# Performance work log

Measured on AMD Instinct MI355X. Metric: run time of the kernel, lower is better.

Reference implementation:

```python
import jax, jax.numpy as jnp
import numpy as np

N_NODES = 100_000
N_EDGES = 3_200_000
D_IN, D_EDGE, D_HID, D_OUT = 8, 4, 32, 16
NEG_SLOPE = 0.2  # PyG GATv2Conv default


def setup_inputs() -> dict:
    key = jax.random.key(0)
    ks = jax.random.split(key, 13)
    s = 0.1
    return {
        "x": jax.random.normal(ks[0], (N_NODES, D_IN), jnp.float32),
        "edge_index": jax.random.randint(ks[1], (2, N_EDGES), 0, N_NODES, dtype=jnp.int64),
        "edge_attr": jax.random.normal(ks[2], (N_EDGES, D_EDGE), jnp.float32),
        "Wl1": jax.random.normal(ks[3], (D_IN, D_HID), jnp.float32) * s,
        "Wr1": jax.random.normal(ks[4], (D_IN, D_HID), jnp.float32) * s,
        "We1": jax.random.normal(ks[5], (D_EDGE, D_HID), jnp.float32) * s,
        "att1": jax.random.normal(ks[6], (D_HID,), jnp.float32) * s,
        "b1": jnp.zeros((D_HID,), jnp.float32),
        "Wl2": jax.random.normal(ks[7], (D_HID, D_OUT), jnp.float32) * s,
        "Wr2": jax.random.normal(ks[8], (D_HID, D_OUT), jnp.float32) * s,
        "We2": jax.random.normal(ks[9], (D_EDGE, D_OUT), jnp.float32) * s,
        "att2": jax.random.normal(ks[10], (D_OUT,), jnp.float32) * s,
        "b2": jnp.zeros((D_OUT,), jnp.float32),
    }


def _segment_softmax(score, seg, n):
    m = jax.ops.segment_max(score, seg, num_segments=n)
    e = jnp.exp(score - m[seg])
    z = jax.ops.segment_sum(e, seg, num_segments=n)
    return e / z[seg]


def _gatv2(x, src, dst, ea_raw, Wl, Wr, We, att, bias, n):
    # GATv2 (heads=1): score_ij = att . leaky_relu(Wl x_j + Wr x_i + We e_ij)
    xl = x @ Wl            # [N, d]
    xr = x @ Wr            # [N, d]
    ea = ea_raw @ We       # [E, d]
    h = jax.nn.leaky_relu(xl[src] + xr[dst] + ea, NEG_SLOPE)  # [E, d]
    score = h @ att        # [E]
    alpha = _segment_softmax(score, dst, n)
    out = jax.ops.segment_sum(alpha[:, None] * xl[src], dst, num_segments=n)
    return out + bias


def reference(x, edge_index, edge_attr, Wl1, Wr1, We1, att1, b1, Wl2, Wr2, We2, att2, b2):
    n = x.shape[0]
    src, dst = edge_index[0], edge_index[1]
    # add_self_loops=True with fill_value='mean': self-loop edge_attr = mean of
    # incoming raw edge_attr per target node (0 for isolated targets)
    ones = jnp.ones((src.shape[0],), x.dtype)
    cnt = jax.ops.segment_sum(ones, dst, num_segments=n)
    loop_attr = jax.ops.segment_sum(edge_attr, dst, num_segments=n) / jnp.maximum(cnt, 1.0)[:, None]
    ar = jnp.arange(n, dtype=src.dtype)
    src2 = jnp.concatenate([src, ar])
    dst2 = jnp.concatenate([dst, ar])
    ea2 = jnp.concatenate([edge_attr, loop_attr], axis=0)
    h = jax.nn.relu(_gatv2(x, src2, dst2, ea2, Wl1, Wr1, We1, att1, b1, n))
    out = _gatv2(h, src2, dst2, ea2, Wl2, Wr2, We2, att2, b2, n)
    return out.reshape(-1)
```

## Files before the change

kernel.cpp:

```cpp
#include <hip/hip_runtime.h>

#define NEG_SLOPE 0.2f
#define CHUNK 16384
#define KMAX  1600
#define CAP   3264
#define NBLKMAX 256

__global__ __launch_bounds__(1024) void k_bin(const int* __restrict__ ei,
                                              const float* __restrict__ eattr,
                                              int* __restrict__ cloff,
                                              int* __restrict__ ssrc,
                                              float4* __restrict__ seat,
                                              int E, int K) {
    __shared__ int s_off[KMAX + 1];
    __shared__ unsigned s_eid[CHUNK];
    int t = threadIdx.x;
    for (int i = t; i <= K; i += 1024) s_off[i] = 0;
    __syncthreads();
    int base = blockIdx.x * CHUNK;
    int end = min(base + CHUNK, E);
    int Ec = end - base;
    unsigned pack[CHUNK / 1024];
#pragma unroll
    for (int i = 0; i < CHUNK / 1024; i++) {
        int el = t + 1024 * i;
        pack[i] = 0xFFFFFFFFu;
        if (el < Ec) {
            int dst = ei[E + base + el];
            int b = dst >> 6;
            int r = atomicAdd(&s_off[b], 1);
            pack[i] = ((unsigned)b << 20) | ((unsigned)(dst & 63) << 14) | (unsigned)r;
        }
    }
    __syncthreads();
    if (t < 64) {
        int run = 0;
        for (int bb = 0; bb < K; bb += 64) {
            int b = bb + t;
            int v = (b < K) ? s_off[b] : 0;
            int x = v;
#pragma unroll
            for (int off = 1; off < 64; off <<= 1) {
                int y = __shfl_up(x, off, 64);
                if (t >= off) x += y;
            }
            if (b < K) s_off[b] = run + x - v;
            run += __shfl(x, 63, 64);
        }
        if (t == 0) s_off[K] = run;
    }
    __syncthreads();
#pragma unroll
    for (int i = 0; i < CHUNK / 1024; i++) {
        int el = t + 1024 * i;
        if (el < Ec) {
            unsigned p = pack[i];
            int b = p >> 20;
            int r = p & 0x3FFF;
            int dl = (p >> 14) & 63;
            s_eid[s_off[b] + r] = ((unsigned)dl << 14) | (unsigned)el;
        }
    }
    __syncthreads();
    for (int pos = t; pos < Ec; pos += 1024) {
        unsigned v = s_eid[pos];
        int el = v & 0x3FFF;
        int dl = v >> 14;
        int e = base + el;
        int src = ei[e];
        float4 a = *(const float4*)(eattr + 4ll * e);
        ssrc[base + pos] = src | (dl << 17);
        seat[base + pos] = a;
    }
    for (int i = t; i <= K; i += 1024)
        cloff[(long long)blockIdx.x * (K + 1) + i] = s_off[i];
}

__global__ void k_transp(const int* __restrict__ in, int* __restrict__ out, int R, int C) {
    __shared__ int tile[32][33];
    int c0 = blockIdx.x * 32, r0 = blockIdx.y * 32;
    int c = c0 + threadIdx.x, r = r0 + threadIdx.y;
    if (r < R && c < C) tile[threadIdx.y][threadIdx.x] = in[(long long)r * C + c];
    __syncthreads();
    int oc = r0 + threadIdx.x, orr = c0 + threadIdx.y;
    if (orr < C && oc < R) out[(long long)orr * R + oc] = tile[threadIdx.x][threadIdx.y];
}

__global__ void k_btot(const int* __restrict__ cloffT, int* __restrict__ bucketTotal,
                       int K, int NBLK) {
    int b = (blockIdx.x * blockDim.x + threadIdx.x) >> 6;
    int lane = threadIdx.x & 63;
    if (b >= K) return;
    const int* r0 = cloffT + (long long)b * NBLK;
    const int* r1 = r0 + NBLK;
    int s = 0;
    for (int c = lane; c < NBLK; c += 64) s += r1[c] - r0[c];
#pragma unroll
    for (int off = 32; off >= 1; off >>= 1) s += __shfl_xor(s, off, 64);
    if (lane == 0) bucketTotal[b] = s;
}

__global__ void k_scanK(const int* __restrict__ bucketTotal, int* __restrict__ slotBase,
                        int* __restrict__ start, int N, int K) {
    __shared__ int s[512];
    int t = threadIdx.x;
    int v[4];
    int sum = 0;
    int base = t * 4;
    for (int j = 0; j < 4; j++) {
        int b = base + j, x = 0;
        if (b < K) { int nb = min(64, N - (b << 6)); x = bucketTotal[b] + nb; }
        v[j] = sum;
        sum += x;
    }
    s[t] = sum;
    __syncthreads();
    for (int off = 1; off < 512; off <<= 1) {
        int x = (t >= off) ? s[t - off] : 0;
        __syncthreads();
        s[t] += x;
        __syncthreads();
    }
    int tb = s[t] - sum;
    for (int j = 0; j < 4; j++) {
        int b = base + j;
        if (b < K) slotBase[b] = tb + v[j];
    }
    if (t == 511) { slotBase[K] = s[511]; start[N] = s[511]; }
}

__global__ __launch_bounds__(512, 8) void k_perm(const int* __restrict__ ssrc,
                                                 const float4* __restrict__ seat,
                                                 const int* __restrict__ cloffT,
                                                 const int* __restrict__ slotBase,
                                                 int* __restrict__ start,
                                                 int* __restrict__ fsrc,
                                                 float4* __restrict__ feat,
                                                 int N, int K, int NBLK) {
    __shared__ int s_pack[CAP];
    __shared__ int s_g[CAP];
    __shared__ int co[NBLKMAX], qq[NBLKMAX + 1], sc[NBLKMAX];
    __shared__ int hist[64], cur[64], lstart[64];
    __shared__ float lsum[64][4];
    int b = blockIdx.x, t = threadIdx.x;
    int nb = min(64, N - (b << 6));
    if (t < 64) {
        hist[t] = 0; cur[t] = 0;
        lsum[t][0] = 0.f; lsum[t][1] = 0.f; lsum[t][2] = 0.f; lsum[t][3] = 0.f;
    }
    const int* r0 = cloffT + (long long)b * NBLK;
    const int* r1 = r0 + NBLK;
    int len = 0;
    if (t < NBLKMAX) {
        if (t < NBLK) { int c0v = r0[t]; len = r1[t] - c0v; co[t] = c0v; }
        sc[t] = (t < NBLK) ? len : 0;
    }
    __syncthreads();
    for (int off = 1; off < NBLKMAX; off <<= 1) {
        int x = 0;
        if (t < NBLKMAX && t >= off) x = sc[t - off];
        __syncthreads();
        if (t < NBLKMAX) sc[t] += x;
        __syncthreads();
    }
    if (t < NBLK) qq[t] = sc[t] - len;
    if (t == NBLKMAX - 1) qq[NBLK] = sc[NBLKMAX - 1];
    __syncthreads();
    int Eb = qq[NBLK];
    for (int i = t; i < Eb; i += 512) {
        int lo2 = 0, hi2 = NBLK;
        while (lo2 + 1 < hi2) { int mid = (lo2 + hi2) >> 1; if (qq[mid] <= i) lo2 = mid; else hi2 = mid; }
        int g = lo2 * CHUNK + co[lo2] + (i - qq[lo2]);
        int p = ssrc[g];
        s_pack[i] = p;
        s_g[i] = g;
        atomicAdd(&hist[(p >> 17) & 63], 1);
    }
    __syncthreads();
    if (t < 64) {
        int v = (t < nb) ? hist[t] + 1 : 0;
        int x = v;
#pragma unroll
        for (int off = 1; off < 64; off <<= 1) {
            int y = __shfl_up(x, off, 64);
            if (t >= off) x += y;
        }
        lstart[t] = x - v;
        if (t < nb) start[(b << 6) + t] = slotBase[b] + lstart[t];
    }
    __syncthreads();
    int lo = slotBase[b];
    for (int i = t; i < Eb; i += 512) {
        int p = s_pack[i];
        int dl = (p >> 17) & 63;
        int src = p & 0x1FFFF;
        int r = atomicAdd(&cur[dl], 1);
        float4 a = seat[s_g[i]];
        long long pos = lo + lstart[dl] + 1 + r;
        fsrc[pos] = src;
        feat[pos] = a;
        atomicAdd(&lsum[dl][0], a.x);
        atomicAdd(&lsum[dl][1], a.y);
        atomicAdd(&lsum[dl][2], a.z);
        atomicAdd(&lsum[dl][3], a.w);
    }
    __syncthreads();
    if (t < nb) {
        float inv = 1.f / fmaxf((float)hist[t], 1.f);
        long long pos = lo + lstart[t];
        fsrc[pos] = (b << 6) + t;
        feat[pos] = make_float4(lsum[t][0] * inv, lsum[t][1] * inv,
                                lsum[t][2] * inv, lsum[t][3] * inv);
    }
}

template <int DIN, int D>
__global__ void k_xform(const float* __restrict__ x, const float* __restrict__ Wl,
                        const float* __restrict__ Wr, float* __restrict__ xl,
                        float* __restrict__ xr, int N) {
    __shared__ float sWl[DIN * D], sWr[DIN * D];
    for (int i = threadIdx.x; i < DIN * D; i += blockDim.x) { sWl[i] = Wl[i]; sWr[i] = Wr[i]; }
    __syncthreads();
    int t = blockIdx.x * blockDim.x + threadIdx.x;
    if (t >= N * D) return;
    int n = t / D, d = t % D;
    const float* xp = x + (long long)n * DIN;
    float sl = 0.f, sr = 0.f;
#pragma unroll
    for (int k = 0; k < DIN; k++) {
        float xv = xp[k];
        sl += xv * sWl[k * D + d];
        sr += xv * sWr[k * D + d];
    }
    xl[t] = sl;
    xr[t] = sr;
}

template <int D, bool RELU>
__global__ void k_gat(const int* __restrict__ fsrc, const float4* __restrict__ feat,
                      const int* __restrict__ start,
                      const float* __restrict__ xl, const float* __restrict__ xr,
                      const float* __restrict__ We, const float* __restrict__ att,
                      const float* __restrict__ bias, float* __restrict__ out, int N) {
    constexpr int L = D / 4;
    constexpr int G = 64 / L;
    int w = (blockIdx.x * blockDim.x + threadIdx.x) >> 6;
    int lane = threadIdx.x & 63;
    if (w >= N) return;
    int g = lane / L;
    int j = lane % L;
    int s0 = start[w], s1 = start[w + 1];

    const float4 we0 = *(const float4*)(We + 0 * D + 4 * j);
    const float4 we1 = *(const float4*)(We + 1 * D + 4 * j);
    const float4 we2 = *(const float4*)(We + 2 * D + 4 * j);
    const float4 we3 = *(const float4*)(We + 3 * D + 4 * j);
    const float4 av  = *(const float4*)(att + 4 * j);
    const float4 xrv = *(const float4*)(xr + (long long)w * D + 4 * j);

    float4 acc = make_float4(0.f, 0.f, 0.f, 0.f);
    float z = 0.f;

    for (int slot = s0 + g; slot < s1; slot += G) {
        int src = fsrc[slot];
        float4 a = feat[slot];
        float4 xlv = *(const float4*)(xl + (long long)src * D + 4 * j);
        float4 v;
        v.x = xlv.x + xrv.x + a.x * we0.x + a.y * we1.x + a.z * we2.x + a.w * we3.x;
        v.y = xlv.y + xrv.y + a.x * we0.y + a.y * we1.y + a.z * we2.y + a.w * we3.y;
        v.z = xlv.z + xrv.z + a.x * we0.z + a.y * we1.z + a.z * we2.z + a.w * we3.z;
        v.w = xlv.w + xrv.w + a.x * we0.w + a.y * we1.w + a.z * we2.w + a.w * we3.w;
        v.x = v.x > 0.f ? v.x : NEG_SLOPE * v.x;
        v.y = v.y > 0.f ? v.y : NEG_SLOPE * v.y;
        v.z = v.z > 0.f ? v.z : NEG_SLOPE * v.z;
        v.w = v.w > 0.f ? v.w : NEG_SLOPE * v.w;
        float sc2 = av.x * v.x + av.y * v.y + av.z * v.z + av.w * v.w;
#pragma unroll
        for (int off = L / 2; off >= 1; off >>= 1) sc2 += __shfl_xor(sc2, off, 64);
        float ev = __expf(sc2);
        z += ev;
        acc.x += ev * xlv.x;
        acc.y += ev * xlv.y;
        acc.z += ev * xlv.z;
        acc.w += ev * xlv.w;
    }

#pragma unroll
    for (int off = 32; off >= L; off >>= 1) {
        acc.x += __shfl_xor(acc.x, off, 64);
        acc.y += __shfl_xor(acc.y, off, 64);
        acc.z += __shfl_xor(acc.z, off, 64);
        acc.w += __shfl_xor(acc.w, off, 64);
        z += __shfl_xor(z, off, 64);
    }

    if (g == 0) {
        float inv = 1.0f / z;
        float4 bv = *(const float4*)(bias + 4 * j);
        float4 o;
        o.x = acc.x * inv + bv.x;
        o.y = acc.y * inv + bv.y;
        o.z = acc.z * inv + bv.z;
        o.w = acc.w * inv + bv.w;
        if (RELU) {
            o.x = fmaxf(o.x, 0.f); o.y = fmaxf(o.y, 0.f);
            o.z = fmaxf(o.z, 0.f); o.w = fmaxf(o.w, 0.f);
        }
        *(float4*)(out + (long long)w * D + 4 * j) = o;
    }
}

extern "C" void kernel_launch(void* const* d_in, const int* in_sizes, int n_in,
                              void* d_out, int out_size, void* d_ws, size_t ws_size,
                              hipStream_t stream) {
    const float* x     = (const float*)d_in[0];
    const int*   ei    = (const int*)d_in[1];
    const float* eattr = (const float*)d_in[2];
    const float* Wl1   = (const float*)d_in[3];
    const float* Wr1   = (const float*)d_in[4];
    const float* We1   = (const float*)d_in[5];
    const float* att1  = (const float*)d_in[6];
    const float* b1    = (const float*)d_in[7];
    const float* Wl2   = (const float*)d_in[8];
    const float* Wr2   = (const float*)d_in[9];
    const float* We2   = (const float*)d_in[10];
    const float* att2  = (const float*)d_in[11];
    const float* b2    = (const float*)d_in[12];

    const int N = in_sizes[0] / 8;
    const int E = in_sizes[1] / 2;
    const int K = (N + 63) >> 6;
    const int NBLK = (E + CHUNK - 1) / CHUNK;

    int* iws = (int*)d_ws;
    size_t o = 0;
    int* bucketTotal = iws + o; o += K;
    int* slotBase    = iws + o; o += K + 1;
    int* start       = iws + o; o += N + 1;
    int* cloff       = iws + o; o += (size_t)NBLK * (K + 1);
    int* cloffT      = iws + o; o += (size_t)(K + 1) * NBLK;
    o = (o + 7) & ~(size_t)7;
    int*    fsrc = (int*)(iws + o);    o += (size_t)(E + N);
    o = (o + 3) & ~(size_t)3;
    float4* feat = (float4*)(iws + o); o += 4ll * (E + N);
    size_t stage = o;
    int*    ssrc = (int*)(iws + o);    o += (size_t)E;
    o = (o + 3) & ~(size_t)3;
    float4* seat = (float4*)(iws + o); o += 4ll * E;
    float* xl = (float*)(iws + stage);
    float* xr = xl + 32ll * N;
    float* h  = xr + 32ll * N;

    const int B = 256;
    auto cdiv = [](long long a, long long b) { return (int)((a + b - 1) / b); };

    k_bin<<<NBLK, 1024, 0, stream>>>(ei, eattr, cloff, ssrc, seat, E, K);
    dim3 tb(32, 32);
    k_transp<<<dim3(cdiv(K + 1, 32), cdiv(NBLK, 32)), tb, 0, stream>>>(cloff, cloffT, NBLK, K + 1);
    k_btot<<<cdiv(64ll * K, B), B, 0, stream>>>(cloffT, bucketTotal, K, NBLK);
    k_scanK<<<1, 512, 0, stream>>>(bucketTotal, slotBase, start, N, K);
    k_perm<<<K, 512, 0, stream>>>(ssrc, seat, cloffT, slotBase, start, fsrc, feat, N, K, NBLK);

    k_xform<8, 32><<<cdiv(32ll * N, B), B, 0, stream>>>(x, Wl1, Wr1, xl, xr, N);
    k_gat<32, true><<<cdiv(N, 4), B, 0, stream>>>(fsrc, feat, start, xl, xr, We1, att1, b1, h, N);

    k_xform<32, 16><<<cdiv(16ll * N, B), B, 0, stream>>>(h, Wl2, Wr2, xl, xr, N);
    k_gat<16, false><<<cdiv(N, 4), B, 0, stream>>>(fsrc, feat, start, xl, xr, We2, att2, b2, (float*)d_out, N);
}
```

Before: 495.9 us.

## Fuse edge permutation into per-bucket GAT kernels with shared-memory atomic accumulation

Drops the CSR build (bucket totals, global scan, permutation into fsrc/feat). Each layer now runs one bucket-level kernel: a block handles 64 destination nodes and streams their binned edges straight from the k_bin staging arrays. The xr projection, per-destination sums and self-loop mean are computed in shared memory, and the softmax numerator and denominator are accumulated with LDS float atomics. This avoids writing and re-reading the permuted edge arrays and cuts the launch count. In exchange it repeats the binary-search edge lookup in each layer, and atomic contention on 64 rows may serialize.

```diff
diff --git a/kernel.cpp b/kernel.cpp
--- a/kernel.cpp
+++ b/kernel.cpp
@@ -3,7 +3,6 @@
 #define NEG_SLOPE 0.2f
 #define CHUNK 16384
 #define KMAX  1600
-#define CAP   3264
 #define NBLKMAX 256
 
 __global__ __launch_bounds__(1024) void k_bin(const int* __restrict__ ei,
@@ -86,68 +85,51 @@
     if (orr < C && oc < R) out[(long long)orr * R + oc] = tile[threadIdx.x][threadIdx.y];
 }
 
-__global__ void k_btot(const int* __restrict__ cloffT, int* __restrict__ bucketTotal,
-                       int K, int NBLK) {
-    int b = (blockIdx.x * blockDim.x + threadIdx.x) >> 6;
-    int lane = threadIdx.x & 63;
-    if (b >= K) return;
-    const int* r0 = cloffT + (long long)b * NBLK;
-    const int* r1 = r0 + NBLK;
-    int s = 0;
-    for (int c = lane; c < NBLK; c += 64) s += r1[c] - r0[c];
-#pragma unroll
-    for (int off = 32; off >= 1; off >>= 1) s += __shfl_xor(s, off, 64);
-    if (lane == 0) bucketTotal[b] = s;
-}
-
-__global__ void k_scanK(const int* __restrict__ bucketTotal, int* __restrict__ slotBase,
-                        int* __restrict__ start, int N, int K) {
-    __shared__ int s[512];
-    int t = threadIdx.x;
-    int v[4];
-    int sum = 0;
-    int base = t * 4;
-    for (int j = 0; j < 4; j++) {
-        int b = base + j, x = 0;
-        if (b < K) { int nb = min(64, N - (b << 6)); x = bucketTotal[b] + nb; }
-        v[j] = sum;
-        sum += x;
-    }
-    s[t] = sum;
-    __syncthreads();
-    for (int off = 1; off < 512; off <<= 1) {
-        int x = (t >= off) ? s[t - off] : 0;
-        __syncthreads();
-        s[t] += x;
-        __syncthreads();
-    }
-    int tb = s[t] - sum;
-    for (int j = 0; j < 4; j++) {
-        int b = base + j;
-        if (b < K) slotBase[b] = tb + v[j];
-    }
-    if (t == 511) { slotBase[K] = s[511]; start[N] = s[511]; }
-}
-
-__global__ __launch_bounds__(512, 8) void k_perm(const int* __restrict__ ssrc,
+template <int DIN, int D>
+__global__ void k_xlform(const float* __restrict__ x, const float* __restrict__ Wl,
+                         float* __restrict__ xl, int N) {
+    __shared__ float sWl[DIN * D];
+    for (int i = threadIdx.x; i < DIN * D; i += blockDim.x) sWl[i] = Wl[i];
+    __syncthreads();
+    int t = blockIdx.x * blockDim.x + threadIdx.x;
+    if (t >= N * D) return;
+    int n = t / D, d = t % D;
+    const float* xp = x + (long long)n * DIN;
+    float sl = 0.f;
+#pragma unroll
+    for (int k = 0; k < DIN; k++) sl += xp[k] * sWl[k * D + d];
+    xl[t] = sl;
+}
+
+template <int D, int DIN, bool RELU>
+__global__ __launch_bounds__(512, 6) void k_gatb(const int* __restrict__ ssrc,
                                                  const float4* __restrict__ seat,
                                                  const int* __restrict__ cloffT,
-                                                 const int* __restrict__ slotBase,
-                                                 int* __restrict__ start,
-                                                 int* __restrict__ fsrc,
-                                                 float4* __restrict__ feat,
+                                                 const float* __restrict__ xt,
+                                                 const float* __restrict__ xin,
+                                                 const float* __restrict__ Wr,
+                                                 const float* __restrict__ We,
+                                                 const float* __restrict__ att,
+                                                 const float* __restrict__ bias,
+                                                 float* __restrict__ out,
                                                  int N, int K, int NBLK) {
-    __shared__ int s_pack[CAP];
-    __shared__ int s_g[CAP];
+    constexpr int L = D / 4;
+    constexpr int NGRP = 512 / L;
+    constexpr int PD = D + 4;
+    __shared__ float s_xr[64][PD];
+    __shared__ float s_acc[64][PD];
+    __shared__ float s_z[64], s_lsum[64][4];
+    __shared__ int s_hist[64];
+    __shared__ float s_Wr[DIN * D];
     __shared__ int co[NBLKMAX], qq[NBLKMAX + 1], sc[NBLKMAX];
-    __shared__ int hist[64], cur[64], lstart[64];
-    __shared__ float lsum[64][4];
     int b = blockIdx.x, t = threadIdx.x;
     int nb = min(64, N - (b << 6));
+    for (int i = t; i < 64 * D; i += 512) s_acc[i / D][i % D] = 0.f;
     if (t < 64) {
-        hist[t] = 0; cur[t] = 0;
-        lsum[t][0] = 0.f; lsum[t][1] = 0.f; lsum[t][2] = 0.f; lsum[t][3] = 0.f;
-    }
+        s_z[t] = 0.f; s_hist[t] = 0;
+        s_lsum[t][0] = 0.f; s_lsum[t][1] = 0.f; s_lsum[t][2] = 0.f; s_lsum[t][3] = 0.f;
+    }
+    for (int i = t; i < DIN * D; i += 512) s_Wr[i] = Wr[i];
     const int* r0 = cloffT + (long long)b * NBLK;
     const int* r1 = r0 + NBLK;
     int len = 0;
@@ -156,115 +138,43 @@
         sc[t] = (t < NBLK) ? len : 0;
     }
     __syncthreads();
+    for (int idx = t; idx < 64 * D; idx += 512) {
+        int q = idx / D, d = idx % D;
+        float s = 0.f;
+        if (q < nb) {
+            const float* xp = xin + (long long)((b << 6) + q) * DIN;
+#pragma unroll
+            for (int k2 = 0; k2 < DIN; k2++) s += xp[k2] * s_Wr[k2 * D + d];
+        }
+        s_xr[q][d] = s;
+    }
     for (int off = 1; off < NBLKMAX; off <<= 1) {
-        int x = 0;
-        if (t < NBLKMAX && t >= off) x = sc[t - off];
+        int x2 = 0;
+        if (t < NBLKMAX && t >= off) x2 = sc[t - off];
         __syncthreads();
-        if (t < NBLKMAX) sc[t] += x;
+        if (t < NBLKMAX) sc[t] += x2;
         __syncthreads();
     }
     if (t < NBLK) qq[t] = sc[t] - len;
     if (t == NBLKMAX - 1) qq[NBLK] = sc[NBLKMAX - 1];
     __syncthreads();
     int Eb = qq[NBLK];
-    for (int i = t; i < Eb; i += 512) {
-        int lo2 = 0, hi2 = NBLK;
-        while (lo2 + 1 < hi2) { int mid = (lo2 + hi2) >> 1; if (qq[mid] <= i) lo2 = mid; else hi2 = mid; }
-        int g = lo2 * CHUNK + co[lo2] + (i - qq[lo2]);
-        int p = ssrc[g];
-        s_pack[i] = p;
-        s_g[i] = g;
-        atomicAdd(&hist[(p >> 17) & 63], 1);
-    }
-    __syncthreads();
-    if (t < 64) {
-        int v = (t < nb) ? hist[t] + 1 : 0;
-        int x = v;
-#pragma unroll
-        for (int off = 1; off < 64; off <<= 1) {
-            int y = __shfl_up(x, off, 64);
-            if (t >= off) x += y;
-        }
-        lstart[t] = x - v;
-        if (t < nb) start[(b << 6) + t] = slotBase[b] + lstart[t];
-    }
-    __syncthreads();
-    int lo = slotBase[b];
-    for (int i = t; i < Eb; i += 512) {
-        int p = s_pack[i];
-        int dl = (p >> 17) & 63;
-        int src = p & 0x1FFFF;
-        int r = atomicAdd(&cur[dl], 1);
-        float4 a = seat[s_g[i]];
-        long long pos = lo + lstart[dl] + 1 + r;
-        fsrc[pos] = src;
-        feat[pos] = a;
-        atomicAdd(&lsum[dl][0], a.x);
-        atomicAdd(&lsum[dl][1], a.y);
-        atomicAdd(&lsum[dl][2], a.z);
-        atomicAdd(&lsum[dl][3], a.w);
-    }
-    __syncthreads();
-    if (t < nb) {
-        float inv = 1.f / fmaxf((float)hist[t], 1.f);
-        long long pos = lo + lstart[t];
-        fsrc[pos] = (b << 6) + t;
-        feat[pos] = make_float4(lsum[t][0] * inv, lsum[t][1] * inv,
-                                lsum[t][2] * inv, lsum[t][3] * inv);
-    }
-}
-
-template <int DIN, int D>
-__global__ void k_xform(const float* __restrict__ x, const float* __restrict__ Wl,
-                        const float* __restrict__ Wr, float* __restrict__ xl,
-                        float* __restrict__ xr, int N) {
-    __shared__ float sWl[DIN * D], sWr[DIN * D];
-    for (int i = threadIdx.x; i < DIN * D; i += blockDim.x) { sWl[i] = Wl[i]; sWr[i] = Wr[i]; }
-    __syncthreads();
-    int t = blockIdx.x * blockDim.x + threadIdx.x;
-    if (t >= N * D) return;
-    int n = t / D, d = t % D;
-    const float* xp = x + (long long)n * DIN;
-    float sl = 0.f, sr = 0.f;
-#pragma unroll
-    for (int k = 0; k < DIN; k++) {
-        float xv = xp[k];
-        sl += xv * sWl[k * D + d];
-        sr += xv * sWr[k * D + d];
-    }
-    xl[t] = sl;
-    xr[t] = sr;
-}
-
-template <int D, bool RELU>
-__global__ void k_gat(const int* __restrict__ fsrc, const float4* __restrict__ feat,
-                      const int* __restrict__ start,
-                      const float* __restrict__ xl, const float* __restrict__ xr,
-                      const float* __restrict__ We, const float* __restrict__ att,
-                      const float* __restrict__ bias, float* __restrict__ out, int N) {
-    constexpr int L = D / 4;
-    constexpr int G = 64 / L;
-    int w = (blockIdx.x * blockDim.x + threadIdx.x) >> 6;
-    int lane = threadIdx.x & 63;
-    if (w >= N) return;
-    int g = lane / L;
-    int j = lane % L;
-    int s0 = start[w], s1 = start[w + 1];
-
+    int grp = t / L, j = t % L;
     const float4 we0 = *(const float4*)(We + 0 * D + 4 * j);
     const float4 we1 = *(const float4*)(We + 1 * D + 4 * j);
     const float4 we2 = *(const float4*)(We + 2 * D + 4 * j);
     const float4 we3 = *(const float4*)(We + 3 * D + 4 * j);
     const float4 av  = *(const float4*)(att + 4 * j);
-    const float4 xrv = *(const float4*)(xr + (long long)w * D + 4 * j);
-
-    float4 acc = make_float4(0.f, 0.f, 0.f, 0.f);
-    float z = 0.f;
-
-    for (int slot = s0 + g; slot < s1; slot += G) {
-        int src = fsrc[slot];
-        float4 a = feat[slot];
-        float4 xlv = *(const float4*)(xl + (long long)src * D + 4 * j);
+    for (int i = grp; i < Eb; i += NGRP) {
+        int lo2 = 0, hi2 = NBLK;
+        while (lo2 + 1 < hi2) { int mid = (lo2 + hi2) >> 1; if (qq[mid] <= i) lo2 = mid; else hi2 = mid; }
+        int g = lo2 * CHUNK + co[lo2] + (i - qq[lo2]);
+        int p = ssrc[g];
+        int src = p & 0x1FFFF;
+        int dl = (p >> 17) & 63;
+        float4 a = seat[g];
+        float4 xlv = *(const float4*)(xt + (long long)src * D + 4 * j);
+        float4 xrv = *(const float4*)(&s_xr[dl][4 * j]);
         float4 v;
         v.x = xlv.x + xrv.x + a.x * we0.x + a.y * we1.x + a.z * we2.x + a.w * we3.x;
         v.y = xlv.y + xrv.y + a.x * we0.y + a.y * we1.y + a.z * we2.y + a.w * we3.y;
@@ -278,35 +188,55 @@
 #pragma unroll
         for (int off = L / 2; off >= 1; off >>= 1) sc2 += __shfl_xor(sc2, off, 64);
         float ev = __expf(sc2);
-        z += ev;
-        acc.x += ev * xlv.x;
-        acc.y += ev * xlv.y;
-        acc.z += ev * xlv.z;
-        acc.w += ev * xlv.w;
-    }
-
-#pragma unroll
-    for (int off = 32; off >= L; off >>= 1) {
-        acc.x += __shfl_xor(acc.x, off, 64);
-        acc.y += __shfl_xor(acc.y, off, 64);
-        acc.z += __shfl_xor(acc.z, off, 64);
-        acc.w += __shfl_xor(acc.w, off, 64);
-        z += __shfl_xor(z, off, 64);
-    }
-
-    if (g == 0) {
-        float inv = 1.0f / z;
-        float4 bv = *(const float4*)(bias + 4 * j);
-        float4 o;
-        o.x = acc.x * inv + bv.x;
-        o.y = acc.y * inv + bv.y;
-        o.z = acc.z * inv + bv.z;
-        o.w = acc.w * inv + bv.w;
-        if (RELU) {
-            o.x = fmaxf(o.x, 0.f); o.y = fmaxf(o.y, 0.f);
-            o.z = fmaxf(o.z, 0.f); o.w = fmaxf(o.w, 0.f);
-        }
-        *(float4*)(out + (long long)w * D + 4 * j) = o;
+        if (j == 0) {
+            atomicAdd(&s_z[dl], ev);
+            atomicAdd(&s_hist[dl], 1);
+            atomicAdd(&s_lsum[dl][0], a.x);
+            atomicAdd(&s_lsum[dl][1], a.y);
+            atomicAdd(&s_lsum[dl][2], a.z);
+            atomicAdd(&s_lsum[dl][3], a.w);
+        }
+        atomicAdd(&s_acc[dl][4 * j + 0], ev * xlv.x);
+        atomicAdd(&s_acc[dl][4 * j + 1], ev * xlv.y);
+        atomicAdd(&s_acc[dl][4 * j + 2], ev * xlv.z);
+        atomicAdd(&s_acc[dl][4 * j + 3], ev * xlv.w);
+    }
+    __syncthreads();
+    if (t < 64 * L) {
+        int q = t / L;
+        if (q < nb) {
+            int dst = (b << 6) + q;
+            float inv = 1.f / fmaxf((float)s_hist[q], 1.f);
+            float a0 = s_lsum[q][0] * inv, a1 = s_lsum[q][1] * inv;
+            float a2 = s_lsum[q][2] * inv, a3 = s_lsum[q][3] * inv;
+            float4 xlv = *(const float4*)(xt + (long long)dst * D + 4 * j);
+            float4 xrv = *(const float4*)(&s_xr[q][4 * j]);
+            float4 v;
+            v.x = xlv.x + xrv.x + a0 * we0.x + a1 * we1.x + a2 * we2.x + a3 * we3.x;
+            v.y = xlv.y + xrv.y + a0 * we0.y + a1 * we1.y + a2 * we2.y + a3 * we3.y;
+            v.z = xlv.z + xrv.z + a0 * we0.z + a1 * we1.z + a2 * we2.z + a3 * we3.z;
+            v.w = xlv.w + xrv.w + a0 * we0.w + a1 * we1.w + a2 * we2.w + a3 * we3.w;
+            v.x = v.x > 0.f ? v.x : NEG_SLOPE * v.x;
+            v.y = v.y > 0.f ? v.y : NEG_SLOPE * v.y;
+            v.z = v.z > 0.f ? v.z : NEG_SLOPE * v.z;
+            v.w = v.w > 0.f ? v.w : NEG_SLOPE * v.w;
+            float sc2 = av.x * v.x + av.y * v.y + av.z * v.z + av.w * v.w;
+#pragma unroll
+            for (int off = L / 2; off >= 1; off >>= 1) sc2 += __shfl_xor(sc2, off, 64);
+            float ev = __expf(sc2);
+            float zinv = 1.f / (s_z[q] + ev);
+            float4 bv = *(const float4*)(bias + 4 * j);
+            float4 o;
+            o.x = (s_acc[q][4 * j + 0] + ev * xlv.x) * zinv + bv.x;
+            o.y = (s_acc[q][4 * j + 1] + ev * xlv.y) * zinv + bv.y;
+            o.z = (s_acc[q][4 * j + 2] + ev * xlv.z) * zinv + bv.z;
+            o.w = (s_acc[q][4 * j + 3] + ev * xlv.w) * zinv + bv.w;
+            if (RELU) {
+                o.x = fmaxf(o.x, 0.f); o.y = fmaxf(o.y, 0.f);
+                o.z = fmaxf(o.z, 0.f); o.w = fmaxf(o.w, 0.f);
+            }
+            *(float4*)(out + (long long)dst * D + 4 * j) = o;
+        }
     }
 }
 
@@ -334,22 +264,15 @@
 
     int* iws = (int*)d_ws;
     size_t o = 0;
-    int* bucketTotal = iws + o; o += K;
-    int* slotBase    = iws + o; o += K + 1;
-    int* start       = iws + o; o += N + 1;
-    int* cloff       = iws + o; o += (size_t)NBLK * (K + 1);
-    int* cloffT      = iws + o; o += (size_t)(K + 1) * NBLK;
-    o = (o + 7) & ~(size_t)7;
-    int*    fsrc = (int*)(iws + o);    o += (size_t)(E + N);
+    int* cloff  = iws + o; o += (size_t)NBLK * (K + 1);
+    int* cloffT = iws + o; o += (size_t)(K + 1) * NBLK;
     o = (o + 3) & ~(size_t)3;
-    float4* feat = (float4*)(iws + o); o += 4ll * (E + N);
-    size_t stage = o;
     int*    ssrc = (int*)(iws + o);    o += (size_t)E;
     o = (o + 3) & ~(size_t)3;
     float4* seat = (float4*)(iws + o); o += 4ll * E;
-    float* xl = (float*)(iws + stage);
-    float* xr = xl + 32ll * N;
-    float* h  = xr + 32ll * N;
+    float* xl1 = (float*)(iws + o);    o += 32ll * N;
+    float* h   = (float*)(iws + o);    o += 32ll * N;
+    float* xl2 = xl1;
 
     const int B = 256;
     auto cdiv = [](long long a, long long b) { return (int)((a + b - 1) / b); };
@@ -357,13 +280,12 @@
     k_bin<<<NBLK, 1024, 0, stream>>>(ei, eattr, cloff, ssrc, seat, E, K);
     dim3 tb(32, 32);
     k_transp<<<dim3(cdiv(K + 1, 32), cdiv(NBLK, 32)), tb, 0, stream>>>(cloff, cloffT, NBLK, K + 1);
-    k_btot<<<cdiv(64ll * K, B), B, 0, stream>>>(cloffT, bucketTotal, K, NBLK);
-    k_scanK<<<1, 512, 0, stream>>>(bucketTotal, slotBase, start, N, K);
-    k_perm<<<K, 512, 0, stream>>>(ssrc, seat, cloffT, slotBase, start, fsrc, feat, N, K, NBLK);
-
-    k_xform<8, 32><<<cdiv(32ll * N, B), B, 0, stream>>>(x, Wl1, Wr1, xl, xr, N);
-    k_gat<32, true><<<cdiv(N, 4), B, 0, stream>>>(fsrc, feat, start, xl, xr, We1, att1, b1, h, N);
-
-    k_xform<32, 16><<<cdiv(16ll * N, B), B, 0, stream>>>(h, Wl2, Wr2, xl, xr, N);
-    k_gat<16, false><<<cdiv(N, 4), B, 0, stream>>>(fsrc, feat, start, xl, xr, We2, att2, b2, (float*)d_out, N);
-}
+
+    k_xlform<8, 32><<<cdiv(32ll * N, B), B, 0, stream>>>(x, Wl1, xl1, N);
+    k_gatb<32, 8, true><<<K, 512, 0, stream>>>(ssrc, seat, cloffT, xl1, x, Wr1,
+                                               We1, att1, b1, h, N, K, NBLK);
+
+    k_xlform<32, 16><<<cdiv(16ll * N, B), B, 0, stream>>>(h, Wl2, xl2, N);
+    k_gatb<16, 32, false><<<K, 512, 0, stream>>>(ssrc, seat, cloffT, xl2, h, Wr2,
+                                                 We2, att2, b2, (float*)d_out, N, K, NBLK);
+}
```

Result: slower. 1.378 ms (+177.8%).
